# Kernel tuning notes

Hardware: AMD Instinct MI355X
Metric: run time of the kernel (lower is better)

## Reference

```python
import jax, jax.numpy as jnp
import numpy as np

ALPHA = 0.2       # LeakyReLU negative slope
OUT_FEATURES = 256
NEG_INF = -9e15   # matches -9000000000000000.0 in the torch code

N = 8192
IN_FEATURES = 512


def setup_inputs() -> dict:
    key = jax.random.key(0)
    k1, k2, k3, k4 = jax.random.split(key, 4)
    h = jax.random.normal(k1, (N, IN_FEATURES), dtype=jnp.float32)
    adj = jax.random.randint(k2, (N, N), 0, 2, dtype=jnp.int32)
    # xavier-uniform-like init scales (exact init values don't matter for correctness)
    W = jax.random.normal(k3, (IN_FEATURES, OUT_FEATURES), dtype=jnp.float32) * 0.05
    a = jax.random.normal(k4, (2 * OUT_FEATURES, 1), dtype=jnp.float32) * 0.05
    return {"h": h, "adj": adj, "W": W, "a": a, "split_name": 0}


def reference(h, adj, W, a, split_name):
    # h: [N, Fin], W: [Fin, Fout], a: [2*Fout, 1], adj: [N, N]
    Wh = h @ W                                   # [N, Fout]
    Wh1 = Wh @ a[:OUT_FEATURES, :]               # [N, 1]
    Wh2 = Wh @ a[OUT_FEATURES:, :]               # [N, 1]
    e = jax.nn.leaky_relu(Wh1 + Wh2.T, negative_slope=ALPHA)  # [N, N]
    mask = adj > 0
    scores = jnp.where(mask, e, jnp.float32(NEG_INF))
    attention = jax.nn.softmax(scores, axis=1)
    # dropout is identity in eval mode (training=False)
    attention = jnp.where(mask, attention, jnp.float32(0.0))
    h_prime = attention @ Wh                     # [N, Fout]
    return jax.nn.elu(h_prime)                   # concat=True -> elu
```

## Files before the change

kernel.cpp:

```cpp
#include <hip/hip_runtime.h>

#define NN 8192
#define FIN 512
#define FOUT 256
#define JS 8
#define STRIP 1024
#define NSTEP 32

typedef _Float16 f16;
typedef __attribute__((ext_vector_type(8))) _Float16 f16x8;
typedef __attribute__((ext_vector_type(4))) _Float16 f16x4;
typedef __attribute__((ext_vector_type(4))) float f32x4;
typedef __attribute__((ext_vector_type(16))) float f32x16;
typedef __attribute__((ext_vector_type(4))) int i32x4;
typedef unsigned long long u64;

__device__ __forceinline__ float lrelu(float x) { return fmaxf(x, 0.2f * x); }

__global__ void k_convert(const int* __restrict__ adj, u64* __restrict__ maskG) {
  int gw = blockIdx.x * 4 + (threadIdx.x >> 6);
  int l = threadIdx.x & 63;
  const int* src = adj + (size_t)gw * NN + 4 * l;
  u64* dst = maskG + (size_t)gw * 128;
  i32x4 v[4];
#pragma unroll
  for (int p = 0; p < 4; ++p)
    v[p] = __builtin_nontemporal_load((const i32x4*)(src + p * 256));
#pragma unroll 1
  for (int p = 0; p < 32; ++p) {
    i32x4 cur = v[p & 3];
    u64 b0 = __ballot(cur[0] > 0);
    u64 b1 = __ballot(cur[1] > 0);
    u64 b2 = __ballot(cur[2] > 0);
    u64 b3 = __ballot(cur[3] > 0);
    if (p + 4 < 32)
      v[p & 3] = __builtin_nontemporal_load((const i32x4*)(src + (p + 4) * 256));
    if (l < 4) {
      u64 bb = (l == 0) ? b0 : (l == 1) ? b1 : (l == 2) ? b2 : b3;
      dst[p * 4 + l] = bb;
    }
  }
}

__global__ void k_prep_w(const float* __restrict__ W, f16* __restrict__ wth,
                         f16* __restrict__ wtl) {
  int id = blockIdx.x * 256 + threadIdx.x;
  int c = id >> 9, k = id & 511;
  float v = W[k * FOUT + c];
  f16 a = (f16)v;
  wth[c * FIN + k] = a;
  wtl[c * FIN + k] = (f16)(v - (float)a);
}

__launch_bounds__(256, 2)
__global__ void k_gemm1(const float* __restrict__ h, const f16* __restrict__ wth,
                        const f16* __restrict__ wtl, const float* __restrict__ avec,
                        f16* __restrict__ whT16, float* __restrict__ wh1,
                        float* __restrict__ wh2) {
  int i0 = blockIdx.x * 32;
  int tid = threadIdx.x;
  int w = tid >> 6, l = tid & 63, m = l & 15, g = l >> 4;
  f32x4 acc[2][4] = {};
#pragma unroll 1
  for (int k0 = 0; k0 < FIN; k0 += 32) {
    f16x8 ah[2], al[2], bh[4], bl[4];
#pragma unroll
    for (int rf = 0; rf < 2; ++rf) {
      int ro = (i0 + 16 * rf + m) * FIN + k0 + 8 * g;
      f32x4 va = *(const f32x4*)(h + ro);
      f32x4 vb = *(const f32x4*)(h + ro + 4);
#pragma unroll
      for (int e = 0; e < 4; ++e) {
        f16 x = (f16)va[e];
        ah[rf][e] = x;
        al[rf][e] = (f16)(va[e] - (float)x);
        f16 y = (f16)vb[e];
        ah[rf][4 + e] = y;
        al[rf][4 + e] = (f16)(vb[e] - (float)y);
      }
    }
#pragma unroll
    for (int cf = 0; cf < 4; ++cf) {
      int co = (64 * w + 16 * cf + m) * FIN + k0 + 8 * g;
      bh[cf] = *(const f16x8*)(wth + co);
      bl[cf] = *(const f16x8*)(wtl + co);
    }
#pragma unroll
    for (int rf = 0; rf < 2; ++rf)
#pragma unroll
      for (int cf = 0; cf < 4; ++cf) {
        acc[rf][cf] = __builtin_amdgcn_mfma_f32_16x16x32_f16(ah[rf], bh[cf], acc[rf][cf], 0, 0, 0);
        acc[rf][cf] = __builtin_amdgcn_mfma_f32_16x16x32_f16(ah[rf], bl[cf], acc[rf][cf], 0, 0, 0);
        acc[rf][cf] = __builtin_amdgcn_mfma_f32_16x16x32_f16(al[rf], bh[cf], acc[rf][cf], 0, 0, 0);
      }
  }
  __shared__ float tile[32][FOUT + 1];
#pragma unroll
  for (int rf = 0; rf < 2; ++rf)
#pragma unroll
    for (int cf = 0; cf < 4; ++cf)
#pragma unroll
      for (int r = 0; r < 4; ++r)
        tile[16 * rf + 4 * g + r][64 * w + 16 * cf + m] = acc[rf][cf][r];
  __syncthreads();
  {
    int c = tid;
    f16x8 vv[4];
#pragma unroll
    for (int r = 0; r < 32; ++r) vv[r >> 3][r & 7] = (f16)tile[r][c];
    size_t base = ((size_t)(i0 >> 4) * 256 + c) * 16;
    *(f16x8*)(whT16 + base) = vv[0];
    *(f16x8*)(whT16 + base + 8) = vv[1];
    *(f16x8*)(whT16 + base + 4096) = vv[2];
    *(f16x8*)(whT16 + base + 4096 + 8) = vv[3];
  }
  {
    int r = tid >> 3, ls = tid & 7;
    float s1 = 0.f, s2 = 0.f;
    for (int c = ls; c < FOUT; c += 8) {
      float v = tile[r][c];
      s1 = fmaf(v, avec[c], s1);
      s2 = fmaf(v, avec[FOUT + c], s2);
    }
#pragma unroll
    for (int off = 1; off < 8; off <<= 1) {
      s1 += __shfl_xor(s1, off);
      s2 += __shfl_xor(s2, off);
    }
    if (ls == 0) {
      wh1[i0 + r] = s1;
      wh2[i0 + r] = s2;
    }
  }
}

__global__ void k_maxprep(const float* __restrict__ wh1, const float* __restrict__ wh2,
                          float* __restrict__ e1p, float* __restrict__ e1n,
                          float* __restrict__ thr, float* __restrict__ e2p,
                          float* __restrict__ e2n) {
  int t = threadIdx.x;
  float mx = -1e30f;
  for (int i = t; i < NN; i += 256) mx = fmaxf(mx, wh2[i]);
#pragma unroll
  for (int off = 1; off < 64; off <<= 1) mx = fmaxf(mx, __shfl_xor(mx, off));
  __shared__ float sm[4];
  if ((t & 63) == 0) sm[t >> 6] = mx;
  __syncthreads();
  float M2 = fmaxf(fmaxf(sm[0], sm[1]), fmaxf(sm[2], sm[3]));
  const float L = 1.4426950408889634f;
  int i = blockIdx.x * 256 + t;
  float w1 = wh1[i], w2 = wh2[i];
  float m = lrelu(w1 + M2);
  e1p[i] = exp2f((w1 - m) * L);
  e1n[i] = exp2f((0.2f * w1 - m) * L);
  thr[i] = exp2f(-w1 * L);
  e2p[i] = exp2f(w2 * L);
  e2n[i] = exp2f(0.2f * w2 * L);
}

__launch_bounds__(256, 2)
__global__ void k_attn(const u64* __restrict__ maskG, const f16* __restrict__ whT16,
                       const float* __restrict__ e1pA, const float* __restrict__ e1nA,
                       const float* __restrict__ thrA, const float* __restrict__ e2pA,
                       const float* __restrict__ e2nA, f16* __restrict__ accP,
                       float* __restrict__ zP) {
  int bx = blockIdx.x;
  int js = bx & (JS - 1), rb = bx >> 3;
  int i0b = rb * 128;
  int jbase = js * STRIP;
  int tid = threadIdx.x, w = tid >> 6, l = tid & 63;
  int lr = l & 31, hi = l >> 5;
  int row = i0b + w * 32 + lr;

  __shared__ u64 mrow[4][32][18];
  __shared__ __align__(16) char ldsB[2][16384];

#pragma unroll
  for (int p = 0; p < 4; ++p) {
    int r = 8 * p + (l >> 3);
    const i32x4* src =
        (const i32x4*)(maskG + (size_t)(i0b + 32 * w + r) * 128 + js * 16) + (l & 7);
    *(i32x4*)(&mrow[w][r][(l & 7) * 2]) = *src;
  }

  float E1p = e1pA[row], E1n = e1nA[row], T = thrA[row];
  f32x16 acc[8] = {};
  float za = 0.f;

  const size_t jb16 = (size_t)(jbase >> 4) * 4096;
  const float* e2pb = e2pA + jbase + 8 * hi;
  const float* e2nb = e2nA + jbase + 8 * hi;

  int ldst[4];
  size_t gsrc[4];
#pragma unroll
  for (int r = 0; r < 4; ++r) {
    int g = r * 256 + tid;
    gsrc[r] = (size_t)(g >> 9) * 4096 + 8 * (g & 511);
    ldst[r] = (g >> 9) * 8192 + ((16 * (g & 511)) ^ (((g >> 3) & 7) << 4));
  }
  int rdbase = (lr * 32 + hi * 16) ^ (((lr >> 2) & 7) << 4);

  i32x4 stg[4];
#pragma unroll
  for (int r = 0; r < 4; ++r)
    stg[r] = __builtin_nontemporal_load((const i32x4*)(whT16 + jb16 + gsrc[r]));
#pragma unroll
  for (int r = 0; r < 4; ++r) *(i32x4*)(&ldsB[0][ldst[r]]) = stg[r];
  __syncthreads();

#pragma unroll 1
  for (int ch = 0; ch < 4; ++ch) {
    u64 wr0[4];
#pragma unroll
    for (int q = 0; q < 4; ++q) wr0[q] = mrow[w][lr][ch * 4 + q];
#pragma unroll 1
    for (int ts = 0; ts < 8; ++ts) {
      int t = ch * 8 + ts;
      int cur = t & 1;
      int jc = t * 32;
      if (t + 1 < NSTEP) {
        const f16* src = whT16 + jb16 + (size_t)(2 * (t + 1)) * 4096;
#pragma unroll
        for (int r = 0; r < 4; ++r)
          stg[r] = __builtin_nontemporal_load((const i32x4*)(src + gsrc[r]));
      }
      int sb = ts * 8 + 2 * hi;
      unsigned b4[4];
#pragma unroll
      for (int e = 0; e < 4; ++e) b4[e] = (unsigned)(wr0[e] >> sb);
      f16x8 pa0, pa1;
#pragma unroll
      for (int q = 0; q < 2; ++q) {
        int fo = jc + 4 * q;
        f32x4 ep0 = *(const f32x4*)(e2pb + fo);
        f32x4 en0 = *(const f32x4*)(e2nb + fo);
        f32x4 ep1 = *(const f32x4*)(e2pb + fo + 16);
        f32x4 en1 = *(const f32x4*)(e2nb + fo + 16);
#pragma unroll
        for (int e = 0; e < 4; ++e) {
          int f = 4 * q + e;
          bool s0 = ep0[e] >= T;
          float v0 = (s0 ? E1p : E1n) * (s0 ? ep0[e] : en0[e]);
          v0 = ((b4[e] >> q) & 1u) ? v0 : 0.f;
          za += v0;
          pa0[f] = (f16)v0;
          bool s1 = ep1[e] >= T;
          float v1 = (s1 ? E1p : E1n) * (s1 ? ep1[e] : en1[e]);
          v1 = ((b4[e] >> (4 + q)) & 1u) ? v1 : 0.f;
          za += v1;
          pa1[f] = (f16)v1;
        }
      }
#pragma unroll
      for (int cf = 0; cf < 8; ++cf) {
        f16x8 bf0 = *(const f16x8*)(&ldsB[cur][cf * 1024 + rdbase]);
        acc[cf] = __builtin_amdgcn_mfma_f32_32x32x16_f16(pa0, bf0, acc[cf], 0, 0, 0);
      }
#pragma unroll
      for (int cf = 0; cf < 8; ++cf) {
        f16x8 bf1 = *(const f16x8*)(&ldsB[cur][8192 + cf * 1024 + rdbase]);
        acc[cf] = __builtin_amdgcn_mfma_f32_32x32x16_f16(pa1, bf1, acc[cf], 0, 0, 0);
      }
      if (t + 1 < NSTEP) {
#pragma unroll
        for (int r = 0; r < 4; ++r) *(i32x4*)(&ldsB[cur ^ 1][ldst[r]]) = stg[r];
        __syncthreads();
      }
    }
  }

  za += __shfl_xor(za, 32);
  if (hi == 0) zP[(size_t)js * NN + row] = za;

  f16* ap = accP + (size_t)js * NN * FOUT;
#pragma unroll
  for (int c = 0; c < 8; ++c)
#pragma unroll
    for (int r = 0; r < 16; ++r) {
      int grow = i0b + 32 * w + (r & 3) + 8 * (r >> 2) + 4 * hi;
      int gcol = c * 32 + lr;
      __builtin_nontemporal_store((f16)acc[c][r], ap + (size_t)grow * FOUT + gcol);
    }
}

__global__ void k_combine(const f16* __restrict__ accP, const float* __restrict__ zP,
                          float* __restrict__ out) {
  int id = blockIdx.x * 256 + threadIdx.x;
  size_t idx = (size_t)id * 4;
  int row = (int)(idx >> 8);
  f32x4 s = {};
#pragma unroll
  for (int p = 0; p < JS; ++p) {
    f16x4 v = *(const f16x4*)(accP + (size_t)p * NN * FOUT + idx);
#pragma unroll
    for (int i = 0; i < 4; ++i) s[i] += (float)v[i];
  }
  float z = 0.f;
#pragma unroll
  for (int p = 0; p < JS; ++p) z += zP[(size_t)p * NN + row];
  float inv = (z > 0.f) ? 1.f / z : 0.f;
  f32x4 o;
#pragma unroll
  for (int i = 0; i < 4; ++i) {
    float x = s[i] * inv;
    o[i] = (x > 0.f) ? x : expm1f(x);
  }
  *(f32x4*)(out + idx) = o;
}

extern "C" void kernel_launch(void* const* d_in, const int* in_sizes, int n_in,
                              void* d_out, int out_size, void* d_ws, size_t ws_size,
                              hipStream_t stream) {
  const float* h = (const float*)d_in[0];
  const int* adj = (const int*)d_in[1];
  const float* W = (const float*)d_in[2];
  const float* a = (const float*)d_in[3];
  (void)in_sizes; (void)n_in; (void)out_size; (void)ws_size;

  char* ws = (char*)d_ws;
  size_t off = 0;
  auto alloc = [&](size_t bytes) {
    void* p = ws + off;
    off = (off + bytes + 255) & ~(size_t)255;
    return p;
  };
  f16* accP = (f16*)alloc((size_t)JS * NN * FOUT * 2);
  u64* maskG = (u64*)alloc((size_t)NN * 128 * 8);
  f16* whT16 = (f16*)alloc((size_t)FOUT * NN * 2);
  f16* wth = (f16*)alloc((size_t)FOUT * FIN * 2);
  f16* wtl = (f16*)alloc((size_t)FOUT * FIN * 2);
  float* wh1 = (float*)alloc((size_t)NN * 4);
  float* wh2 = (float*)alloc((size_t)NN * 4);
  float* e1p = (float*)alloc((size_t)NN * 4);
  float* e1n = (float*)alloc((size_t)NN * 4);
  float* thr = (float*)alloc((size_t)NN * 4);
  float* e2p = (float*)alloc((size_t)NN * 4);
  float* e2n = (float*)alloc((size_t)NN * 4);
  float* zP = (float*)alloc((size_t)JS * NN * 4);

  k_convert<<<NN / 4, 256, 0, stream>>>(adj, maskG);
  k_prep_w<<<FIN * FOUT / 256, 256, 0, stream>>>(W, wth, wtl);
  k_gemm1<<<NN / 32, 256, 0, stream>>>(h, wth, wtl, a, whT16, wh1, wh2);
  k_maxprep<<<NN / 256, 256, 0, stream>>>(wh1, wh2, e1p, e1n, thr, e2p, e2n);
  k_attn<<<(NN / 128) * JS, 256, 0, stream>>>(maskG, whT16, e1p, e1n, thr, e2p, e2n,
                                              accP, zP);
  k_combine<<<NN * FOUT / 1024, 256, 0, stream>>>(accP, zP, (float*)d_out);
}
```

Before: 155.8 us.

## Fuse adjacency bitmask conversion into attention kernel via in-loop ballots

Removes the separate k_convert pass that packed the int32 adjacency matrix into a u64 bitmask. The attention kernel now streams the int32 adjacency rows directly, double-buffered two steps ahead in registers, and builds each step's mask bits with wavefront ballots. This drops one kernel launch and the write and re-read of the bitmask buffer. In exchange the attention loop carries 32 extra live registers, more global loads per step and 16 ballots per step, which may hurt occupancy or latency hiding in the MFMA loop.

```diff
diff --git a/kernel.cpp b/kernel.cpp
--- a/kernel.cpp
+++ b/kernel.cpp
@@ -16,31 +16,6 @@
 typedef unsigned long long u64;
 
 __device__ __forceinline__ float lrelu(float x) { return fmaxf(x, 0.2f * x); }
-
-__global__ void k_convert(const int* __restrict__ adj, u64* __restrict__ maskG) {
-  int gw = blockIdx.x * 4 + (threadIdx.x >> 6);
-  int l = threadIdx.x & 63;
-  const int* src = adj + (size_t)gw * NN + 4 * l;
-  u64* dst = maskG + (size_t)gw * 128;
-  i32x4 v[4];
-#pragma unroll
-  for (int p = 0; p < 4; ++p)
-    v[p] = __builtin_nontemporal_load((const i32x4*)(src + p * 256));
-#pragma unroll 1
-  for (int p = 0; p < 32; ++p) {
-    i32x4 cur = v[p & 3];
-    u64 b0 = __ballot(cur[0] > 0);
-    u64 b1 = __ballot(cur[1] > 0);
-    u64 b2 = __ballot(cur[2] > 0);
-    u64 b3 = __ballot(cur[3] > 0);
-    if (p + 4 < 32)
-      v[p & 3] = __builtin_nontemporal_load((const i32x4*)(src + (p + 4) * 256));
-    if (l < 4) {
-      u64 bb = (l == 0) ? b0 : (l == 1) ? b1 : (l == 2) ? b2 : b3;
-      dst[p * 4 + l] = bb;
-    }
-  }
-}
 
 __global__ void k_prep_w(const float* __restrict__ W, f16* __restrict__ wth,
                          f16* __restrict__ wtl) {
@@ -159,7 +134,7 @@
 }
 
 __launch_bounds__(256, 2)
-__global__ void k_attn(const u64* __restrict__ maskG, const f16* __restrict__ whT16,
+__global__ void k_attn(const int* __restrict__ adj, const f16* __restrict__ whT16,
                        const float* __restrict__ e1pA, const float* __restrict__ e1nA,
                        const float* __restrict__ thrA, const float* __restrict__ e2pA,
                        const float* __restrict__ e2nA, f16* __restrict__ accP,
@@ -172,24 +147,17 @@
   int lr = l & 31, hi = l >> 5;
   int row = i0b + w * 32 + lr;
 
-  __shared__ u64 mrow[4][32][18];
   __shared__ __align__(16) char ldsB[2][16384];
-
-#pragma unroll
-  for (int p = 0; p < 4; ++p) {
-    int r = 8 * p + (l >> 3);
-    const i32x4* src =
-        (const i32x4*)(maskG + (size_t)(i0b + 32 * w + r) * 128 + js * 16) + (l & 7);
-    *(i32x4*)(&mrow[w][r][(l & 7) * 2]) = *src;
-  }
 
   float E1p = e1pA[row], E1n = e1nA[row], T = thrA[row];
   f32x16 acc[8] = {};
   float za = 0.f;
 
-  const size_t jb16 = (size_t)(jbase >> 4) * 4096;
+  const f16* bStrip = whT16 + (size_t)(jbase >> 4) * 4096;
   const float* e2pb = e2pA + jbase + 8 * hi;
   const float* e2nb = e2nA + jbase + 8 * hi;
+
+  const int* aSrc = adj + (size_t)(i0b + 32 * w + (l >> 5)) * NN + jbase + (l & 31);
 
   int ldst[4];
   size_t gsrc[4];
@@ -204,69 +172,80 @@
   i32x4 stg[4];
 #pragma unroll
   for (int r = 0; r < 4; ++r)
-    stg[r] = __builtin_nontemporal_load((const i32x4*)(whT16 + jb16 + gsrc[r]));
+    stg[r] = __builtin_nontemporal_load((const i32x4*)(whT16 + (size_t)(jbase >> 4) * 4096 + gsrc[r]));
 #pragma unroll
   for (int r = 0; r < 4; ++r) *(i32x4*)(&ldsB[0][ldst[r]]) = stg[r];
+
+  int pre[2][16];
+#pragma unroll
+  for (int k = 0; k < 16; ++k) {
+    pre[0][k] = __builtin_nontemporal_load(aSrc + (size_t)(2 * k) * NN);
+    pre[1][k] = __builtin_nontemporal_load(aSrc + (size_t)(2 * k) * NN + 32);
+  }
   __syncthreads();
 
 #pragma unroll 1
-  for (int ch = 0; ch < 4; ++ch) {
-    u64 wr0[4];
-#pragma unroll
-    for (int q = 0; q < 4; ++q) wr0[q] = mrow[w][lr][ch * 4 + q];
-#pragma unroll 1
-    for (int ts = 0; ts < 8; ++ts) {
-      int t = ch * 8 + ts;
-      int cur = t & 1;
-      int jc = t * 32;
-      if (t + 1 < NSTEP) {
-        const f16* src = whT16 + jb16 + (size_t)(2 * (t + 1)) * 4096;
-#pragma unroll
-        for (int r = 0; r < 4; ++r)
-          stg[r] = __builtin_nontemporal_load((const i32x4*)(src + gsrc[r]));
+  for (int t = 0; t < NSTEP; ++t) {
+    int cur = t & 1;
+    int jc = t * 32;
+    unsigned b32 = 0;
+#pragma unroll
+    for (int k = 0; k < 16; ++k) {
+      u64 b = __ballot(pre[cur][k] > 0);
+      unsigned mine = (lr & 1) ? (unsigned)(b >> 32) : (unsigned)b;
+      if ((lr >> 1) == k) b32 = mine;
+    }
+    if (t + 2 < NSTEP) {
+#pragma unroll
+      for (int k = 0; k < 16; ++k)
+        pre[cur][k] =
+            __builtin_nontemporal_load(aSrc + (size_t)(2 * k) * NN + (t + 2) * 32);
+    }
+    if (t + 1 < NSTEP) {
+      const f16* src = bStrip + (size_t)(t + 1) * 8192;
+#pragma unroll
+      for (int r = 0; r < 4; ++r)
+        stg[r] = __builtin_nontemporal_load((const i32x4*)(src + gsrc[r]));
+    }
+    unsigned bits0 = (b32 >> (8 * hi)) & 0xFFu;
+    unsigned bits1 = (b32 >> (16 + 8 * hi)) & 0xFFu;
+    f16x8 pa0, pa1;
+#pragma unroll
+    for (int q = 0; q < 2; ++q) {
+      int fo = jc + 4 * q;
+      f32x4 ep0 = *(const f32x4*)(e2pb + fo);
+      f32x4 en0 = *(const f32x4*)(e2nb + fo);
+      f32x4 ep1 = *(const f32x4*)(e2pb + fo + 16);
+      f32x4 en1 = *(const f32x4*)(e2nb + fo + 16);
+#pragma unroll
+      for (int e = 0; e < 4; ++e) {
+        int f = 4 * q + e;
+        bool s0 = ep0[e] >= T;
+        float v0 = (s0 ? E1p : E1n) * (s0 ? ep0[e] : en0[e]);
+        v0 = ((bits0 >> f) & 1u) ? v0 : 0.f;
+        za += v0;
+        pa0[f] = (f16)v0;
+        bool s1 = ep1[e] >= T;
+        float v1 = (s1 ? E1p : E1n) * (s1 ? ep1[e] : en1[e]);
+        v1 = ((bits1 >> f) & 1u) ? v1 : 0.f;
+        za += v1;
+        pa1[f] = (f16)v1;
       }
-      int sb = ts * 8 + 2 * hi;
-      unsigned b4[4];
-#pragma unroll
-      for (int e = 0; e < 4; ++e) b4[e] = (unsigned)(wr0[e] >> sb);
-      f16x8 pa0, pa1;
-#pragma unroll
-      for (int q = 0; q < 2; ++q) {
-        int fo = jc + 4 * q;
-        f32x4 ep0 = *(const f32x4*)(e2pb + fo);
-        f32x4 en0 = *(const f32x4*)(e2nb + fo);
-        f32x4 ep1 = *(const f32x4*)(e2pb + fo + 16);
-        f32x4 en1 = *(const f32x4*)(e2nb + fo + 16);
-#pragma unroll
-        for (int e = 0; e < 4; ++e) {
-          int f = 4 * q + e;
-          bool s0 = ep0[e] >= T;
-          float v0 = (s0 ? E1p : E1n) * (s0 ? ep0[e] : en0[e]);
-          v0 = ((b4[e] >> q) & 1u) ? v0 : 0.f;
-          za += v0;
-          pa0[f] = (f16)v0;
-          bool s1 = ep1[e] >= T;
-          float v1 = (s1 ? E1p : E1n) * (s1 ? ep1[e] : en1[e]);
-          v1 = ((b4[e] >> (4 + q)) & 1u) ? v1 : 0.f;
-          za += v1;
-          pa1[f] = (f16)v1;
-        }
-      }
-#pragma unroll
-      for (int cf = 0; cf < 8; ++cf) {
-        f16x8 bf0 = *(const f16x8*)(&ldsB[cur][cf * 1024 + rdbase]);
-        acc[cf] = __builtin_amdgcn_mfma_f32_32x32x16_f16(pa0, bf0, acc[cf], 0, 0, 0);
-      }
-#pragma unroll
-      for (int cf = 0; cf < 8; ++cf) {
-        f16x8 bf1 = *(const f16x8*)(&ldsB[cur][8192 + cf * 1024 + rdbase]);
-        acc[cf] = __builtin_amdgcn_mfma_f32_32x32x16_f16(pa1, bf1, acc[cf], 0, 0, 0);
-      }
-      if (t + 1 < NSTEP) {
-#pragma unroll
-        for (int r = 0; r < 4; ++r) *(i32x4*)(&ldsB[cur ^ 1][ldst[r]]) = stg[r];
-        __syncthreads();
-      }
+    }
+#pragma unroll
+    for (int cf = 0; cf < 8; ++cf) {
+      f16x8 bf0 = *(const f16x8*)(&ldsB[cur][cf * 1024 + rdbase]);
+      acc[cf] = __builtin_amdgcn_mfma_f32_32x32x16_f16(pa0, bf0, acc[cf], 0, 0, 0);
+    }
+#pragma unroll
+    for (int cf = 0; cf < 8; ++cf) {
+      f16x8 bf1 = *(const f16x8*)(&ldsB[cur][8192 + cf * 1024 + rdbase]);
+      acc[cf] = __builtin_amdgcn_mfma_f32_32x32x16_f16(pa1, bf1, acc[cf], 0, 0, 0);
+    }
+    if (t + 1 < NSTEP) {
+#pragma unroll
+      for (int r = 0; r < 4; ++r) *(i32x4*)(&ldsB[cur ^ 1][ldst[r]]) = stg[r];
+      __syncthreads();
     }
   }
 
@@ -326,7 +305,6 @@
     return p;
   };
   f16* accP = (f16*)alloc((size_t)JS * NN * FOUT * 2);
-  u64* maskG = (u64*)alloc((size_t)NN * 128 * 8);
   f16* whT16 = (f16*)alloc((size_t)FOUT * NN * 2);
   f16* wth = (f16*)alloc((size_t)FOUT * FIN * 2);
   f16* wtl = (f16*)alloc((size_t)FOUT * FIN * 2);
@@ -339,11 +317,10 @@
   float* e2n = (float*)alloc((size_t)NN * 4);
   float* zP = (float*)alloc((size_t)JS * NN * 4);
 
-  k_convert<<<NN / 4, 256, 0, stream>>>(adj, maskG);
   k_prep_w<<<FIN * FOUT / 256, 256, 0, stream>>>(W, wth, wtl);
   k_gemm1<<<NN / 32, 256, 0, stream>>>(h, wth, wtl, a, whT16, wh1, wh2);
   k_maxprep<<<NN / 256, 256, 0, stream>>>(wh1, wh2, e1p, e1n, thr, e2p, e2n);
-  k_attn<<<(NN / 128) * JS, 256, 0, stream>>>(maskG, whT16, e1p, e1n, thr, e2p, e2n,
+  k_attn<<<(NN / 128) * JS, 256, 0, stream>>>(adj, whT16, e1p, e1n, thr, e2p, e2n,
                                               accP, zP);
   k_combine<<<NN * FOUT / 1024, 256, 0, stream>>>(accP, zP, (float*)d_out);
 }
```

Result: slower. 316.7 us (+103.2%).
